# Performance work log

Measured on AMD Instinct MI355X. Metric: run time of the kernel, lower is better.

The kernel has to match this reference:

```python
import jax, jax.numpy as jnp
import numpy as np

IN_SIZE = 1024
OUT_SIZE = 4096
LOGN = 12          # ceil(log2(max(in,out)))
N = 1 << LOGN      # 4096
BATCH = 8192


def setup_inputs() -> dict:
    key = jax.random.key(0)
    k1, k2, k3 = jax.random.split(key, 3)
    # kaiming_uniform on [2*logN, N]: fan_in = N, bound = sqrt(6/fan_in)
    bound = float(np.sqrt(6.0 / N))
    learned_params = jax.random.uniform(k1, (2 * LOGN, N), minval=-bound, maxval=bound, dtype=jnp.float32)
    inp = jax.random.normal(k2, (BATCH, IN_SIZE), dtype=jnp.float32)
    # np.random.permutation(N)[:out_size]
    out_row_indices = jax.random.permutation(k3, N)[:OUT_SIZE].astype(jnp.int32)
    return {"input": inp, "learned_params": learned_params, "out_row_indices": out_row_indices}


def reference(input, learned_params, out_row_indices):
    # Build B = prod_i (diag(p[2i]) + P_i @ diag(p[2i+1])), P_i[j, j^2^i] = 1.
    # (P_i @ diag(d) @ B)[j, :] = d[j^2^i] * B[j^2^i, :], so each layer is a
    # row-scale + xor-permuted row-scale of B (same math as the dense matmul chain).
    B = jnp.eye(N, dtype=input.dtype)
    for i in range(LOGN):
        perm = jnp.arange(N) ^ (1 << i)  # static per layer
        B = learned_params[2 * i][:, None] * B + learned_params[2 * i + 1][perm][:, None] * B[perm]
    layer_matrix = B[out_row_indices, :IN_SIZE]   # [out_size, in_size]
    return input @ layer_matrix.T                  # [batch, out_size]
```

## Files before the change

### kernel.cpp

```cpp
#include <hip/hip_runtime.h>


typedef float f4 __attribute__((ext_vector_type(4)));
typedef int   i4 __attribute__((ext_vector_type(4)));

__device__ __forceinline__ int swz(int e) {
    return e ^ (((e >> 5) & 3) << 2);
}

__global__ void __launch_bounds__(256) bfly_prep(
    const float* __restrict__ lp, const int* __restrict__ orow,
    float* __restrict__ scale, int* __restrict__ src)
{
    int j = blockIdx.x * 256 + threadIdx.x;
    if (j >= 4096) return;
    int r = orow[j];
    int c = r & 1023;
    int u = r & 2047;
    const float* A10 = lp + 20 * 4096;
    const float* B10 = lp + 21 * 4096;
    const float* A11 = lp + 22 * 4096;
    const float* B11 = lp + 23 * 4096;
    float f11 = (r & 2048) ? B11[u] : A11[u];
    float f10 = (r & 1024) ? B10[c] : A10[c];
    scale[j] = f11 * f10;
    src[j] = c;
}

__global__ void __launch_bounds__(256, 2) bfly_main(
    const float* __restrict__ inp, const float* __restrict__ lp,
    const float* __restrict__ scale, const int* __restrict__ src,
    float* __restrict__ out)
{
    __shared__ __align__(16) float cf[12 * 1024];
    const int t = threadIdx.x;
    const int wave = t >> 6, lane = t & 63;

    #pragma unroll
    for (int q = 0; q < 12; ++q) {
        const f4 v = *reinterpret_cast<const f4*>(lp + (size_t)(8 + q) * 4096 + t * 4);
        *reinterpret_cast<f4*>(&cf[q * 1024 + swz(t * 4)]) = v;
    }

    const int sBase = blockIdx.x * 16 + wave * 4;
    float x[4][16];
    #pragma unroll
    for (int m = 0; m < 4; ++m) {
        const f4* p = reinterpret_cast<const f4*>(inp + (size_t)(sBase + m) * 1024 + lane * 16);
        #pragma unroll
        for (int c = 0; c < 4; ++c) {
            f4 v = __builtin_nontemporal_load(p + c);
            x[m][4*c+0] = v.x; x[m][4*c+1] = v.y; x[m][4*c+2] = v.z; x[m][4*c+3] = v.w;
        }
    }

    __syncthreads();

    #pragma unroll
    for (int i = 0; i < 4; ++i) {
        float a[16], b[16];
        const f4* A = reinterpret_cast<const f4*>(lp + (size_t)(2*i)   * 4096 + lane * 16);
        const f4* B = reinterpret_cast<const f4*>(lp + (size_t)(2*i+1) * 4096 + lane * 16);
        #pragma unroll
        for (int c = 0; c < 4; ++c) {
            f4 va = A[c], vb = B[c];
            a[4*c+0]=va.x; a[4*c+1]=va.y; a[4*c+2]=va.z; a[4*c+3]=va.w;
            b[4*c+0]=vb.x; b[4*c+1]=vb.y; b[4*c+2]=vb.z; b[4*c+3]=vb.w;
        }
        const int s = 1 << i;
        #pragma unroll
        for (int m = 0; m < 4; ++m) {
            #pragma unroll
            for (int k = 0; k < 16; ++k) {
                if (!(k & s)) {
                    float lo = x[m][k], hi = x[m][k | s];
                    x[m][k]     = a[k]     * lo + b[k | s] * hi;
                    x[m][k | s] = a[k | s] * hi + b[k]     * lo;
                }
            }
        }
    }

    #pragma unroll
    for (int i = 4; i < 10; ++i) {
        const int d = 1 << (i - 4);
        float a[16], b[16];
        const float* arow = &cf[(size_t)(i - 4) * 2048];
        const float* brow = arow + 1024;
        #pragma unroll
        for (int c = 0; c < 4; ++c) {
            f4 va = *reinterpret_cast<const f4*>(&arow[swz(lane * 16 + 4 * c)]);
            f4 vb = *reinterpret_cast<const f4*>(&brow[swz((lane ^ d) * 16 + 4 * c)]);
            a[4*c+0]=va.x; a[4*c+1]=va.y; a[4*c+2]=va.z; a[4*c+3]=va.w;
            b[4*c+0]=vb.x; b[4*c+1]=vb.y; b[4*c+2]=vb.z; b[4*c+3]=vb.w;
        }
        #pragma unroll
        for (int m = 0; m < 4; ++m) {
            #pragma unroll
            for (int k = 0; k < 16; ++k) {
                float xp = __shfl_xor(x[m][k], d, 64);
                x[m][k] = a[k] * x[m][k] + b[k] * xp;
            }
        }
    }

    __syncthreads();

    float* zw = &cf[(size_t)wave * 2048];
    const i4* srv = reinterpret_cast<const i4*>(src);
    const f4* scv = reinterpret_cast<const f4*>(scale);

    #pragma unroll
    for (int p = 0; p < 2; ++p) {
        #pragma unroll
        for (int h = 0; h < 2; ++h) {
            const float* xr = x[p * 2 + h];
            #pragma unroll
            for (int c = 0; c < 4; ++c) {
                int e = lane * 16 + 4 * c;
                f4 v = { xr[4*c+0], xr[4*c+1], xr[4*c+2], xr[4*c+3] };
                *reinterpret_cast<f4*>(&zw[h * 1024 + swz(e)]) = v;
            }
        }
        #pragma unroll 4
        for (int it = 0; it < 16; ++it) {
            int j4 = it * 64 + lane;
            i4 si = srv[j4];
            f4 sc = scv[j4];
            #pragma unroll
            for (int h = 0; h < 2; ++h) {
                const float* zh = &zw[h * 1024];
                f4 r;
                r.x = sc.x * zh[swz(si.x)];
                r.y = sc.y * zh[swz(si.y)];
                r.z = sc.z * zh[swz(si.z)];
                r.w = sc.w * zh[swz(si.w)];
                __builtin_nontemporal_store(
                    r, reinterpret_cast<f4*>(out + (size_t)(sBase + p * 2 + h) * 4096) + j4);
            }
        }
    }
}

extern "C" void kernel_launch(void* const* d_in, const int* in_sizes, int n_in,
                              void* d_out, int out_size, void* d_ws, size_t ws_size,
                              hipStream_t stream) {
    const float* inp  = (const float*)d_in[0];
    const float* lp   = (const float*)d_in[1];
    const int*   orow = (const int*)d_in[2];
    float* out = (float*)d_out;

    float* scale = (float*)d_ws;
    int*   src   = (int*)((char*)d_ws + 4096 * 4);

    bfly_prep<<<16, 256, 0, stream>>>(lp, orow, scale, src);
    bfly_main<<<512, 256, 0, stream>>>(inp, lp, scale, src, out);
}
```

Before: 50.14 us.

## Split rows into two halves, overlap loads and stores, use DPP for small shuffles

Each wave now processes its four rows as two pairs. The second pair's global loads are issued after the first butterfly setup, so the first pair's output stores can overlap the second pair's computation. A dedicated shared buffer for the gather stage removes the final block-wide barrier. Lane exchanges at distances 1, 2 and 8 use DPP intrinsics instead of ds_bpermute-based shuffles. The extra shared-memory buffer raises LDS usage per block to 80KB, which may limit occupancy. The butterfly coefficients are also reloaded once per half.

```diff
diff --git a/kernel.cpp b/kernel.cpp
--- a/kernel.cpp
+++ b/kernel.cpp
@@ -6,6 +6,13 @@
 
 __device__ __forceinline__ int swz(int e) {
     return e ^ (((e >> 5) & 3) << 2);
+}
+
+template<int CTRL>
+__device__ __forceinline__ float dppx(float x) {
+    int xi = __builtin_bit_cast(int, x);
+    int r  = __builtin_amdgcn_update_dpp(xi, xi, CTRL, 0xF, 0xF, true);
+    return __builtin_bit_cast(float, r);
 }
 
 __global__ void __launch_bounds__(256) bfly_prep(
@@ -33,88 +40,101 @@
     float* __restrict__ out)
 {
     __shared__ __align__(16) float cf[12 * 1024];
+    __shared__ __align__(16) float zbuf[4][2048];
+
     const int t = threadIdx.x;
     const int wave = t >> 6, lane = t & 63;
+    const int sb = blockIdx.x * 16 + wave * 4;
+    float* zw = zbuf[wave];
+
+    float xA[2][16], xB[2][16];
+
+    #pragma unroll
+    for (int m = 0; m < 2; ++m) {
+        const f4* p = reinterpret_cast<const f4*>(inp + (size_t)(sb + m) * 1024 + lane * 16);
+        #pragma unroll
+        for (int c = 0; c < 4; ++c) {
+            f4 v = __builtin_nontemporal_load(p + c);
+            xA[m][4*c+0] = v.x; xA[m][4*c+1] = v.y; xA[m][4*c+2] = v.z; xA[m][4*c+3] = v.w;
+        }
+    }
 
     #pragma unroll
     for (int q = 0; q < 12; ++q) {
         const f4 v = *reinterpret_cast<const f4*>(lp + (size_t)(8 + q) * 4096 + t * 4);
         *reinterpret_cast<f4*>(&cf[q * 1024 + swz(t * 4)]) = v;
     }
+    __syncthreads();
 
-    const int sBase = blockIdx.x * 16 + wave * 4;
-    float x[4][16];
     #pragma unroll
-    for (int m = 0; m < 4; ++m) {
-        const f4* p = reinterpret_cast<const f4*>(inp + (size_t)(sBase + m) * 1024 + lane * 16);
+    for (int m = 0; m < 2; ++m) {
+        const f4* p = reinterpret_cast<const f4*>(inp + (size_t)(sb + 2 + m) * 1024 + lane * 16);
         #pragma unroll
         for (int c = 0; c < 4; ++c) {
             f4 v = __builtin_nontemporal_load(p + c);
-            x[m][4*c+0] = v.x; x[m][4*c+1] = v.y; x[m][4*c+2] = v.z; x[m][4*c+3] = v.w;
+            xB[m][4*c+0] = v.x; xB[m][4*c+1] = v.y; xB[m][4*c+2] = v.z; xB[m][4*c+3] = v.w;
         }
     }
 
-    __syncthreads();
-
-    #pragma unroll
-    for (int i = 0; i < 4; ++i) {
-        float a[16], b[16];
-        const f4* A = reinterpret_cast<const f4*>(lp + (size_t)(2*i)   * 4096 + lane * 16);
-        const f4* B = reinterpret_cast<const f4*>(lp + (size_t)(2*i+1) * 4096 + lane * 16);
+    auto butterfly = [&](float (&x)[2][16]) {
         #pragma unroll
-        for (int c = 0; c < 4; ++c) {
-            f4 va = A[c], vb = B[c];
-            a[4*c+0]=va.x; a[4*c+1]=va.y; a[4*c+2]=va.z; a[4*c+3]=va.w;
-            b[4*c+0]=vb.x; b[4*c+1]=vb.y; b[4*c+2]=vb.z; b[4*c+3]=vb.w;
-        }
-        const int s = 1 << i;
-        #pragma unroll
-        for (int m = 0; m < 4; ++m) {
+        for (int i = 0; i < 4; ++i) {
+            float a[16], b[16];
+            const f4* A = reinterpret_cast<const f4*>(lp + (size_t)(2*i)   * 4096 + lane * 16);
+            const f4* B = reinterpret_cast<const f4*>(lp + (size_t)(2*i+1) * 4096 + lane * 16);
             #pragma unroll
-            for (int k = 0; k < 16; ++k) {
-                if (!(k & s)) {
-                    float lo = x[m][k], hi = x[m][k | s];
-                    x[m][k]     = a[k]     * lo + b[k | s] * hi;
-                    x[m][k | s] = a[k | s] * hi + b[k]     * lo;
+            for (int c = 0; c < 4; ++c) {
+                f4 va = A[c], vb = B[c];
+                a[4*c+0]=va.x; a[4*c+1]=va.y; a[4*c+2]=va.z; a[4*c+3]=va.w;
+                b[4*c+0]=vb.x; b[4*c+1]=vb.y; b[4*c+2]=vb.z; b[4*c+3]=vb.w;
+            }
+            const int s = 1 << i;
+            #pragma unroll
+            for (int m = 0; m < 2; ++m) {
+                #pragma unroll
+                for (int k = 0; k < 16; ++k) {
+                    if (!(k & s)) {
+                        float lo = x[m][k], hi = x[m][k | s];
+                        x[m][k]     = a[k]     * lo + b[k | s] * hi;
+                        x[m][k | s] = a[k | s] * hi + b[k]     * lo;
+                    }
                 }
             }
         }
-    }
-
-    #pragma unroll
-    for (int i = 4; i < 10; ++i) {
-        const int d = 1 << (i - 4);
-        float a[16], b[16];
-        const float* arow = &cf[(size_t)(i - 4) * 2048];
-        const float* brow = arow + 1024;
         #pragma unroll
-        for (int c = 0; c < 4; ++c) {
-            f4 va = *reinterpret_cast<const f4*>(&arow[swz(lane * 16 + 4 * c)]);
-            f4 vb = *reinterpret_cast<const f4*>(&brow[swz((lane ^ d) * 16 + 4 * c)]);
-            a[4*c+0]=va.x; a[4*c+1]=va.y; a[4*c+2]=va.z; a[4*c+3]=va.w;
-            b[4*c+0]=vb.x; b[4*c+1]=vb.y; b[4*c+2]=vb.z; b[4*c+3]=vb.w;
-        }
-        #pragma unroll
-        for (int m = 0; m < 4; ++m) {
+        for (int i = 4; i < 10; ++i) {
+            const int d = 1 << (i - 4);
+            float a[16], b[16];
+            const float* arow = &cf[(size_t)(i - 4) * 2048];
+            const float* brow = arow + 1024;
             #pragma unroll
-            for (int k = 0; k < 16; ++k) {
-                float xp = __shfl_xor(x[m][k], d, 64);
-                x[m][k] = a[k] * x[m][k] + b[k] * xp;
+            for (int c = 0; c < 4; ++c) {
+                f4 va = *reinterpret_cast<const f4*>(&arow[swz(lane * 16 + 4 * c)]);
+                f4 vb = *reinterpret_cast<const f4*>(&brow[swz((lane ^ d) * 16 + 4 * c)]);
+                a[4*c+0]=va.x; a[4*c+1]=va.y; a[4*c+2]=va.z; a[4*c+3]=va.w;
+                b[4*c+0]=vb.x; b[4*c+1]=vb.y; b[4*c+2]=vb.z; b[4*c+3]=vb.w;
+            }
+            #pragma unroll
+            for (int m = 0; m < 2; ++m) {
+                #pragma unroll
+                for (int k = 0; k < 16; ++k) {
+                    float xp = (d == 1) ? dppx<0xB1>(x[m][k])
+                             : (d == 2) ? dppx<0x4E>(x[m][k])
+                             : (d == 8) ? dppx<0x128>(x[m][k])
+                             : __shfl_xor(x[m][k], d, 64);
+                    x[m][k] = a[k] * x[m][k] + b[k] * xp;
+                }
             }
         }
-    }
+    };
 
-    __syncthreads();
-
-    float* zw = &cf[(size_t)wave * 2048];
     const i4* srv = reinterpret_cast<const i4*>(src);
     const f4* scv = reinterpret_cast<const f4*>(scale);
 
-    #pragma unroll
-    for (int p = 0; p < 2; ++p) {
+    auto emit = [&](float (&x)[2][16], int s0) {
         #pragma unroll
         for (int h = 0; h < 2; ++h) {
-            const float* xr = x[p * 2 + h];
+            const float* xr = x[h];
             #pragma unroll
             for (int c = 0; c < 4; ++c) {
                 int e = lane * 16 + 4 * c;
@@ -136,10 +156,15 @@
                 r.z = sc.z * zh[swz(si.z)];
                 r.w = sc.w * zh[swz(si.w)];
                 __builtin_nontemporal_store(
-                    r, reinterpret_cast<f4*>(out + (size_t)(sBase + p * 2 + h) * 4096) + j4);
+                    r, reinterpret_cast<f4*>(out + (size_t)(s0 + h) * 4096) + j4);
             }
         }
-    }
+    };
+
+    butterfly(xA);
+    emit(xA, sb);
+    butterfly(xB);
+    emit(xB, sb + 2);
 }
 
 extern "C" void kernel_launch(void* const* d_in, const int* in_sizes, int n_in,
```

Result: slower. 54.40 us (+8.5%).

## Halve rows per wave, use DPP for butterfly exchanges, interleave scatter LDS layout

Applied to the files above, without the earlier changes.

Each wave now processes two input rows instead of four, which doubles the grid and raises launch bounds to four blocks per CU for more occupancy. Layer 8 loads its coefficients from global memory and uses a DPP quad swap. Layers with xor distances 2 and 8 also use DPP instead of ds_bpermute shuffles, and LDS use drops to 10K floats. The output gather interleaves the two rows in LDS with a new swizzle precomputed in the prep kernel, so one 8-byte LDS read serves both rows. The trade-off is that the per-block LDS coefficient load is now amortized over half as many rows.

```diff
diff --git a/kernel.cpp b/kernel.cpp
--- a/kernel.cpp
+++ b/kernel.cpp
@@ -2,15 +2,23 @@
 
 
 typedef float f4 __attribute__((ext_vector_type(4)));
+typedef float f2 __attribute__((ext_vector_type(2)));
 typedef int   i4 __attribute__((ext_vector_type(4)));
 
 __device__ __forceinline__ int swz(int e) {
     return e ^ (((e >> 5) & 3) << 2);
 }
 
+template<int CTRL>
+__device__ __forceinline__ float dppx(float x) {
+    int xi = __builtin_bit_cast(int, x);
+    int r  = __builtin_amdgcn_update_dpp(xi, xi, CTRL, 0xF, 0xF, true);
+    return __builtin_bit_cast(float, r);
+}
+
 __global__ void __launch_bounds__(256) bfly_prep(
     const float* __restrict__ lp, const int* __restrict__ orow,
-    float* __restrict__ scale, int* __restrict__ src)
+    float* __restrict__ scale, int* __restrict__ src2)
 {
     int j = blockIdx.x * 256 + threadIdx.x;
     if (j >= 4096) return;
@@ -24,28 +32,28 @@
     float f11 = (r & 2048) ? B11[u] : A11[u];
     float f10 = (r & 1024) ? B10[c] : A10[c];
     scale[j] = f11 * f10;
-    src[j] = c;
+    src2[j] = c ^ (((c >> 4) & 7) << 1);
 }
 
-__global__ void __launch_bounds__(256, 2) bfly_main(
+__global__ void __launch_bounds__(256, 4) bfly_main(
     const float* __restrict__ inp, const float* __restrict__ lp,
-    const float* __restrict__ scale, const int* __restrict__ src,
+    const float* __restrict__ scale, const int* __restrict__ src2,
     float* __restrict__ out)
 {
-    __shared__ __align__(16) float cf[12 * 1024];
+    __shared__ __align__(16) float cf[10 * 1024];
     const int t = threadIdx.x;
     const int wave = t >> 6, lane = t & 63;
 
     #pragma unroll
-    for (int q = 0; q < 12; ++q) {
-        const f4 v = *reinterpret_cast<const f4*>(lp + (size_t)(8 + q) * 4096 + t * 4);
+    for (int q = 0; q < 10; ++q) {
+        const f4 v = *reinterpret_cast<const f4*>(lp + (size_t)(10 + q) * 4096 + t * 4);
         *reinterpret_cast<f4*>(&cf[q * 1024 + swz(t * 4)]) = v;
     }
 
-    const int sBase = blockIdx.x * 16 + wave * 4;
-    float x[4][16];
+    const int sBase = blockIdx.x * 8 + wave * 2;
+    float x[2][16];
     #pragma unroll
-    for (int m = 0; m < 4; ++m) {
+    for (int m = 0; m < 2; ++m) {
         const f4* p = reinterpret_cast<const f4*>(inp + (size_t)(sBase + m) * 1024 + lane * 16);
         #pragma unroll
         for (int c = 0; c < 4; ++c) {
@@ -69,7 +77,7 @@
         }
         const int s = 1 << i;
         #pragma unroll
-        for (int m = 0; m < 4; ++m) {
+        for (int m = 0; m < 2; ++m) {
             #pragma unroll
             for (int k = 0; k < 16; ++k) {
                 if (!(k & s)) {
@@ -81,11 +89,30 @@
         }
     }
 
+    {
+        float a[16], b[16];
+        const f4* A = reinterpret_cast<const f4*>(lp + (size_t)8 * 4096 + lane * 16);
+        const f4* B = reinterpret_cast<const f4*>(lp + (size_t)9 * 4096 + (lane ^ 1) * 16);
+        #pragma unroll
+        for (int c = 0; c < 4; ++c) {
+            f4 va = A[c], vb = B[c];
+            a[4*c+0]=va.x; a[4*c+1]=va.y; a[4*c+2]=va.z; a[4*c+3]=va.w;
+            b[4*c+0]=vb.x; b[4*c+1]=vb.y; b[4*c+2]=vb.z; b[4*c+3]=vb.w;
+        }
+        #pragma unroll
+        for (int m = 0; m < 2; ++m)
+            #pragma unroll
+            for (int k = 0; k < 16; ++k) {
+                float v = x[m][k];
+                x[m][k] = a[k] * v + b[k] * dppx<0xB1>(v);
+            }
+    }
+
     #pragma unroll
-    for (int i = 4; i < 10; ++i) {
+    for (int i = 5; i < 10; ++i) {
         const int d = 1 << (i - 4);
         float a[16], b[16];
-        const float* arow = &cf[(size_t)(i - 4) * 2048];
+        const float* arow = &cf[(size_t)(i - 5) * 2048];
         const float* brow = arow + 1024;
         #pragma unroll
         for (int c = 0; c < 4; ++c) {
@@ -95,50 +122,47 @@
             b[4*c+0]=vb.x; b[4*c+1]=vb.y; b[4*c+2]=vb.z; b[4*c+3]=vb.w;
         }
         #pragma unroll
-        for (int m = 0; m < 4; ++m) {
+        for (int m = 0; m < 2; ++m) {
             #pragma unroll
             for (int k = 0; k < 16; ++k) {
-                float xp = __shfl_xor(x[m][k], d, 64);
-                x[m][k] = a[k] * x[m][k] + b[k] * xp;
+                float v = x[m][k];
+                float xp = (d == 2) ? dppx<0x4E>(v)
+                         : (d == 8) ? dppx<0x128>(v)
+                         :            __shfl_xor(v, d, 64);
+                x[m][k] = a[k] * v + b[k] * xp;
             }
         }
     }
 
     __syncthreads();
 
-    float* zw = &cf[(size_t)wave * 2048];
-    const i4* srv = reinterpret_cast<const i4*>(src);
-    const f4* scv = reinterpret_cast<const f4*>(scale);
+    float* zz = &cf[(size_t)wave * 2048];
+    const int km0 = (lane & 7) << 1;
 
     #pragma unroll
-    for (int p = 0; p < 2; ++p) {
-        #pragma unroll
-        for (int h = 0; h < 2; ++h) {
-            const float* xr = x[p * 2 + h];
-            #pragma unroll
-            for (int c = 0; c < 4; ++c) {
-                int e = lane * 16 + 4 * c;
-                f4 v = { xr[4*c+0], xr[4*c+1], xr[4*c+2], xr[4*c+3] };
-                *reinterpret_cast<f4*>(&zw[h * 1024 + swz(e)]) = v;
-            }
-        }
-        #pragma unroll 4
-        for (int it = 0; it < 16; ++it) {
-            int j4 = it * 64 + lane;
-            i4 si = srv[j4];
-            f4 sc = scv[j4];
-            #pragma unroll
-            for (int h = 0; h < 2; ++h) {
-                const float* zh = &zw[h * 1024];
-                f4 r;
-                r.x = sc.x * zh[swz(si.x)];
-                r.y = sc.y * zh[swz(si.y)];
-                r.z = sc.z * zh[swz(si.z)];
-                r.w = sc.w * zh[swz(si.w)];
-                __builtin_nontemporal_store(
-                    r, reinterpret_cast<f4*>(out + (size_t)(sBase + p * 2 + h) * 4096) + j4);
-            }
-        }
+    for (int k = 0; k < 16; k += 2) {
+        int pi = lane * 16 + (k ^ km0);
+        f4 v = { x[0][k], x[1][k], x[0][k+1], x[1][k+1] };
+        *reinterpret_cast<f4*>(&zz[2 * pi]) = v;
+    }
+
+    const i4* srv = reinterpret_cast<const i4*>(src2);
+    const f4* scv = reinterpret_cast<const f4*>(scale);
+    float* o0 = out + (size_t)sBase * 4096;
+    float* o1 = out + (size_t)(sBase + 1) * 4096;
+    #pragma unroll 4
+    for (int it = 0; it < 16; ++it) {
+        int j4 = it * 64 + lane;
+        i4 si = srv[j4];
+        f4 sc = scv[j4];
+        f2 vx = *reinterpret_cast<const f2*>(&zz[2 * si.x]);
+        f2 vy = *reinterpret_cast<const f2*>(&zz[2 * si.y]);
+        f2 vz = *reinterpret_cast<const f2*>(&zz[2 * si.z]);
+        f2 vw = *reinterpret_cast<const f2*>(&zz[2 * si.w]);
+        f4 r0 = { sc.x * vx.x, sc.y * vy.x, sc.z * vz.x, sc.w * vw.x };
+        f4 r1 = { sc.x * vx.y, sc.y * vy.y, sc.z * vz.y, sc.w * vw.y };
+        __builtin_nontemporal_store(r0, reinterpret_cast<f4*>(o0) + j4);
+        __builtin_nontemporal_store(r1, reinterpret_cast<f4*>(o1) + j4);
     }
 }
 
@@ -151,8 +175,8 @@
     float* out = (float*)d_out;
 
     float* scale = (float*)d_ws;
-    int*   src   = (int*)((char*)d_ws + 4096 * 4);
+    int*   src2  = (int*)((char*)d_ws + 4096 * 4);
 
-    bfly_prep<<<16, 256, 0, stream>>>(lp, orow, scale, src);
-    bfly_main<<<512, 256, 0, stream>>>(inp, lp, scale, src, out);
+    bfly_prep<<<16, 256, 0, stream>>>(lp, orow, scale, src2);
+    bfly_main<<<1024, 256, 0, stream>>>(inp, lp, scale, src2, out);
 }
```

Measured after the change: 52.51 us. 4.7% more time.
